# Kernel optimization log

Hardware: AMD Instinct MI355X
Metric: run time of the kernel (lower is better)

Reference implementation:

```python
import jax, jax.numpy as jnp
import numpy as np

B, L, D, KSIZE = 8, 2048, 768, 8


def setup_inputs() -> dict:
    key = jax.random.key(0)
    k1, k2, k3, k4, k5 = jax.random.split(key, 5)
    s = 1.0 / np.sqrt(D)  # torch default GRU init scale
    x = jax.random.normal(k1, (B, L, D), dtype=jnp.float32)
    w_ih = jax.random.uniform(k2, (D, 3 * D), jnp.float32, -s, s)
    w_hh = jax.random.uniform(k3, (D, 3 * D), jnp.float32, -s, s)
    b_ih = jax.random.uniform(k4, (3 * D,), jnp.float32, -s, s)
    b_hh = jax.random.uniform(k5, (3 * D,), jnp.float32, -s, s)
    return {"x": x, "w_ih": w_ih, "w_hh": w_hh, "b_ih": b_ih, "b_hh": b_hh, "ksize": KSIZE}


def reference(x, w_ih, w_hh, b_ih, b_hh, ksize):
    """LocalRNN forward: sliding window of size ksize (zero left-pad), GRU over
    each window, return last hidden state per position -> [B, L, D].
    Instead of materializing the redundant [B*L, ksize, D] windowed tensor,
    we run the ksize-step recurrence over all positions in parallel: the j-th
    GRU step for window ending at t consumes xpad[:, t + j, :].
    """
    Bb, Ll, Dd = x.shape
    xpad = jnp.concatenate([jnp.zeros((Bb, ksize - 1, Dd), x.dtype), x], axis=1)
    # precompute input-side gate activations once: [B, L+k-1, 3D]
    gx_all = xpad @ w_ih + b_ih

    def step(h, j):
        gx = jax.lax.dynamic_slice_in_dim(gx_all, j, Ll, axis=1)  # [B, L, 3D]
        gh = h @ w_hh + b_hh                                       # [B, L, 3D]
        xr, xz, xn = jnp.split(gx, 3, axis=-1)
        hr, hz, hn = jnp.split(gh, 3, axis=-1)
        r = jax.nn.sigmoid(xr + hr)
        z = jax.nn.sigmoid(xz + hz)
        n = jnp.tanh(xn + r * hn)
        h_new = (1.0 - z) * n + z * h
        return h_new, None

    h0 = jnp.zeros((Bb, Ll, Dd), x.dtype)
    h, _ = jax.lax.scan(step, h0, jnp.arange(ksize))
    return h
```

## Files before the change

kernel.cpp:

```cpp
#include <hip/hip_runtime.h>
#include <stdint.h>
#include <stddef.h>

using short8 = __attribute__((ext_vector_type(8))) short;
using short4v = __attribute__((ext_vector_type(4))) short;
using f32x4  = __attribute__((ext_vector_type(4))) float;

#define BB 8
#define LL 2048
#define DD 768
#define KS 8
#define ND 2304
#define NT 12
#define NBD 12

__device__ __forceinline__ float bf2f(unsigned short u) {
  union { uint32_t i; float f; } v; v.i = ((uint32_t)u) << 16; return v.f;
}
__device__ __forceinline__ unsigned short f2bf(float f) {
  union { float f; uint32_t i; } v; v.f = f;
  return (unsigned short)((v.i + 0x7FFFu + ((v.i >> 16) & 1u)) >> 16);
}
__device__ __forceinline__ float sigm(float x) { return 1.0f / (1.0f + __expf(-x)); }
__device__ __forceinline__ float tanh_fast(float x) {
  return 2.0f / (1.0f + __expf(-2.0f * x)) - 1.0f;
}
__device__ __forceinline__ void gload_lds16(const void* g, void* lds) {
  __builtin_amdgcn_global_load_lds(
      (const __attribute__((address_space(1))) void*)g,
      (__attribute__((address_space(3))) void*)lds, 16, 0, 0);
}

__device__ __forceinline__ void swz_blocks(int bid, int nbm, int nbn,
                                           int* mb, int* nb) {
  int gsz = 8 * nbn;
  int g = bid / gsz;
  int rem = bid - g * gsz;
  int gg = nbm - g * 8; if (gg > 8) gg = 8;
  *nb = rem / gg;
  *mb = g * 8 + (rem - *nb * gg);
}

__global__ void zero_k(unsigned short* p, int n) {
  int i = blockIdx.x * 256 + threadIdx.x;
  if (i < n) p[i] = 0;
}

__global__ void detect_k(const uint32_t* __restrict__ x, int* __restrict__ flag) {
  int t = threadIdx.x;
  uint32_t w = x[t * 16];
  int e = (int)((w >> 7) & 0xFF);
  int isbf = (e >= 112 && e <= 136) ? 1 : 0;
  unsigned long long m = __ballot(isbf);
  if (t == 0) *flag = (__popcll(m) >= 32) ? 1 : 0;
}

__global__ void transpose_k(const void* __restrict__ in,
                            unsigned short* __restrict__ out, int R, int C,
                            const int* __restrict__ flagp) {
  const bool bf = (*flagp != 0);
  __shared__ unsigned short t[32][33];
  int c0 = blockIdx.x * 32, r0 = blockIdx.y * 32;
  int tx = threadIdx.x, ty = threadIdx.y;
#pragma unroll
  for (int i = ty; i < 32; i += 8) {
    size_t idx = (size_t)(r0 + i) * C + c0 + tx;
    t[i][tx] = bf ? ((const unsigned short*)in)[idx]
                  : f2bf(((const float*)in)[idx]);
  }
  __syncthreads();
#pragma unroll
  for (int i = ty; i < 32; i += 8)
    out[(size_t)(c0 + i) * R + r0 + tx] = t[tx][i];
}

__global__ void conv_bias(const void* __restrict__ in,
                          unsigned short* __restrict__ out, int n,
                          const int* __restrict__ flagp) {
  const bool bf = (*flagp != 0);
  int i = blockIdx.x * 256 + threadIdx.x;
  if (i >= n) return;
  out[i] = bf ? ((const unsigned short*)in)[i] : f2bf(((const float*)in)[i]);
}

__global__ void conv_x(const void* __restrict__ xv,
                       unsigned short* __restrict__ xpadc,
                       int Uc, int t0, int total8,
                       const int* __restrict__ flagp) {
  if (*flagp != 0) return;
  int idx = blockIdx.x * 256 + threadIdx.x;
  if (idx >= total8) return;
  size_t e = (size_t)idx * 8;
  int d = (int)(e % DD);
  size_t ru = e / DD;
  int u = (int)(ru % Uc);
  int b = (int)(ru / Uc);
  int p = t0 + u;
  short8 v = {0, 0, 0, 0, 0, 0, 0, 0};
  if (p >= KS - 1) {
    size_t base = ((size_t)b * LL + (p - (KS - 1))) * DD + d;
    const float* fp = (const float*)xv + base;
    float4 a = *(const float4*)fp, b4 = *(const float4*)(fp + 4);
    v[0] = (short)f2bf(a.x); v[1] = (short)f2bf(a.y);
    v[2] = (short)f2bf(a.z); v[3] = (short)f2bf(a.w);
    v[4] = (short)f2bf(b4.x); v[5] = (short)f2bf(b4.y);
    v[6] = (short)f2bf(b4.z); v[7] = (short)f2bf(b4.w);
  }
  *(short8*)&xpadc[e] = v;
}

__global__ __launch_bounds__(256, 3) void gemm_gx(
    const unsigned short* __restrict__ xbf, const unsigned short* __restrict__ xpadc,
    const unsigned short* __restrict__ zrow, const unsigned short* __restrict__ WT,
    const unsigned short* __restrict__ bih, const unsigned short* __restrict__ bhh,
    unsigned short* __restrict__ gxp, unsigned short* __restrict__ h0,
    int Mrows, int Uc, int Tcc, int t0, const int* __restrict__ flagp, int nbm) {
  __shared__ __align__(16) unsigned short Al[128 * 64];
  __shared__ __align__(16) unsigned short Bl[192 * 64];
  const bool bfm = (*flagp != 0);
  const int tid = threadIdx.x, lane = tid & 63, wv = tid >> 6;
  const int wm = wv >> 1, wd = wv & 1;
  int mb, db; swz_blocks(blockIdx.x, nbm, NBD, &mb, &db);
  const int m0 = mb * 128, d0 = db * 64;
  const int h16 = lane >> 4, l16 = lane & 15;

  const int r0i = tid >> 3;
  const int slotg = (tid & 7) ^ (r0i & 7);
  const unsigned short* asrc[4];
#pragma unroll
  for (int it = 0; it < 4; ++it) {
    int grow = m0 + it * 32 + r0i; if (grow >= Mrows) grow = Mrows - 1;
    if (bfm) {
      int b = grow / Uc, u = grow - b * Uc;
      int p = t0 + u;
      asrc[it] = (p < KS - 1)
          ? (zrow + slotg * 8)
          : (xbf + ((size_t)b * LL + (p - (KS - 1))) * DD + slotg * 8);
    } else {
      asrc[it] = xpadc + (size_t)grow * DD + slotg * 8;
    }
  }
  const unsigned short* bbase = WT + (size_t)(d0 + r0i) * DD + slotg * 8;
  char* aldst = (char*)Al + (wv * 1024);
  char* bldst = (char*)Bl + (wv * 1024);

  f32x4 acc[4][2][3] = {};

  for (int kt = 0; kt < NT; ++kt) {
    const int ko = kt * 64;
#pragma unroll
    for (int it = 0; it < 4; ++it)
      gload_lds16(asrc[it] + ko, aldst + it * 4096);
#pragma unroll
    for (int it = 0; it < 6; ++it) {
      const size_t boff = (size_t)(it >> 1) * (DD * DD) + (size_t)(it & 1) * (32 * DD);
      gload_lds16(bbase + boff + ko, bldst + it * 4096);
    }
    __syncthreads();
#pragma unroll
    for (int s = 0; s < 2; ++s) {
      short8 af[4];
#pragma unroll
      for (int i = 0; i < 4; ++i) {
        int row = wm * 64 + i * 16 + l16;
        af[i] = *(const short8*)&Al[row * 64 + (((s * 4 + h16) ^ (row & 7)) * 8)];
      }
      short8 bfr[2][3];
#pragma unroll
      for (int jd = 0; jd < 2; ++jd)
#pragma unroll
        for (int g = 0; g < 3; ++g) {
          int row = g * 64 + wd * 32 + jd * 16 + l16;
          bfr[jd][g] = *(const short8*)&Bl[row * 64 + (((s * 4 + h16) ^ (row & 7)) * 8)];
        }
#pragma unroll
      for (int i = 0; i < 4; ++i)
#pragma unroll
        for (int jd = 0; jd < 2; ++jd)
#pragma unroll
          for (int g = 0; g < 3; ++g)
            acc[i][jd][g] = __builtin_amdgcn_mfma_f32_16x16x32_bf16(af[i], bfr[jd][g], acc[i][jd][g], 0, 0, 0);
    }
    if (kt + 1 < NT) __syncthreads();
  }

  const int b0 = m0 / Uc;
  const int u00 = m0 - b0 * Uc;
#pragma unroll
  for (int jd = 0; jd < 2; ++jd) {
    int d = d0 + wd * 32 + jd * 16 + l16;
    float bir = bf2f(bih[d]), biz = bf2f(bih[DD + d]), bin_ = bf2f(bih[2 * DD + d]);
    float bhr = bf2f(bhh[d]), bhz = bf2f(bhh[DD + d]), bhn = bf2f(bhh[2 * DD + d]);
#pragma unroll
    for (int i = 0; i < 4; ++i) {
      int mbase = m0 + wm * 64 + i * 16 + 4 * h16;
#pragma unroll
      for (int r2 = 0; r2 < 4; ++r2) {
        int m = mbase + r2;
        if (m >= Mrows) continue;
        float gr = acc[i][jd][0][r2] + bir;
        float gz = acc[i][jd][1][r2] + biz;
        float gn = acc[i][jd][2][r2] + bin_;
        short4v pk;
        pk[0] = (short)f2bf(gr); pk[1] = (short)f2bf(gz);
        pk[2] = (short)f2bf(gn); pk[3] = 0;
        *(short4v*)(gxp + (size_t)m * (DD * 4) + d * 4) = pk;
        int uu = u00 + (m - m0);
        int b = b0;
        if (uu >= Uc) { b += 1; uu -= Uc; }
        if (uu < Tcc) {
          float r = sigm(gr + bhr);
          float z = sigm(gz + bhz);
          float n = tanh_fast(gn + r * bhn);
          h0[((size_t)b * Tcc + uu) * DD + d] = f2bf((1.0f - z) * n);
        }
      }
    }
  }
}

__global__ __launch_bounds__(256, 3) void gemm_gru_step(
    const unsigned short* __restrict__ Hc, const unsigned short* __restrict__ WT,
    const unsigned short* __restrict__ bhh, const unsigned short* __restrict__ gxp,
    int Uc, void* __restrict__ Hn, int hnBS, int hnOff, int j, int lgTc,
    const int* __restrict__ flagp, int isFinal, int nbm) {
  __shared__ __align__(16) unsigned short Al[128 * 64];
  __shared__ __align__(16) unsigned short Bl[192 * 64];
  const bool bfm = (*flagp != 0);
  const int tid = threadIdx.x, lane = tid & 63, wv = tid >> 6;
  const int wm = wv >> 1, wd = wv & 1;
  int mb, db; swz_blocks(blockIdx.x, nbm, NBD, &mb, &db);
  const int m0 = mb * 128, d0 = db * 64;
  const int h16 = lane >> 4, l16 = lane & 15;
  const int tmask = (1 << lgTc) - 1;

  const int r0i = tid >> 3;
  const int slotg = (tid & 7) ^ (r0i & 7);
  const unsigned short* abase = Hc + (size_t)(m0 + r0i) * DD + slotg * 8;
  const unsigned short* bbase = WT + (size_t)(d0 + r0i) * DD + slotg * 8;
  char* aldst = (char*)Al + (wv * 1024);
  char* bldst = (char*)Bl + (wv * 1024);

  f32x4 acc[4][2][3] = {};

  for (int kt = 0; kt < NT; ++kt) {
    const int ko = kt * 64;
#pragma unroll
    for (int it = 0; it < 4; ++it)
      gload_lds16(abase + (size_t)it * (32 * DD) + ko, aldst + it * 4096);
#pragma unroll
    for (int it = 0; it < 6; ++it) {
      const size_t boff = (size_t)(it >> 1) * (DD * DD) + (size_t)(it & 1) * (32 * DD);
      gload_lds16(bbase + boff + ko, bldst + it * 4096);
    }
    __syncthreads();
#pragma unroll
    for (int s = 0; s < 2; ++s) {
      short8 af[4];
#pragma unroll
      for (int i = 0; i < 4; ++i) {
        int row = wm * 64 + i * 16 + l16;
        af[i] = *(const short8*)&Al[row * 64 + (((s * 4 + h16) ^ (row & 7)) * 8)];
      }
      short8 bfr[2][3];
#pragma unroll
      for (int jd = 0; jd < 2; ++jd)
#pragma unroll
        for (int g = 0; g < 3; ++g) {
          int row = g * 64 + wd * 32 + jd * 16 + l16;
          bfr[jd][g] = *(const short8*)&Bl[row * 64 + (((s * 4 + h16) ^ (row & 7)) * 8)];
        }
#pragma unroll
      for (int i = 0; i < 4; ++i)
#pragma unroll
        for (int jd = 0; jd < 2; ++jd)
#pragma unroll
          for (int g = 0; g < 3; ++g)
            acc[i][jd][g] = __builtin_amdgcn_mfma_f32_16x16x32_bf16(af[i], bfr[jd][g], acc[i][jd][g], 0, 0, 0);
    }
    if (kt + 1 < NT) __syncthreads();
  }

#pragma unroll
  for (int jd = 0; jd < 2; ++jd) {
    int d = d0 + wd * 32 + jd * 16 + l16;
    float br = bf2f(bhh[d]), bz = bf2f(bhh[DD + d]), bn = bf2f(bhh[2 * DD + d]);
#pragma unroll
    for (int i = 0; i < 4; ++i) {
      int mbase = m0 + wm * 64 + i * 16 + 4 * h16;
#pragma unroll
      for (int r2 = 0; r2 < 4; ++r2) {
        int m = mbase + r2;
        int b = m >> lgTc, t = m & tmask;
        size_t gxrow = (size_t)b * Uc + t + j;
        short4v pk = *(const short4v*)(gxp + gxrow * (DD * 4) + d * 4);
        float xr = bf2f((unsigned short)pk[0]);
        float xz = bf2f((unsigned short)pk[1]);
        float xn = bf2f((unsigned short)pk[2]);
        float gr = acc[i][jd][0][r2] + br;
        float gz = acc[i][jd][1][r2] + bz;
        float gn = acc[i][jd][2][r2] + bn;
        float rr = sigm(xr + gr);
        float zz = sigm(xz + gz);
        float nn = tanh_fast(xn + rr * gn);
        float ho = bf2f(Hc[(size_t)m * DD + d]);
        float val = (1.0f - zz) * nn + zz * ho;
        size_t hnrow = (size_t)b * hnBS + hnOff + t;
        if (isFinal && !bfm) ((float*)Hn)[hnrow * DD + d] = val;
        else ((unsigned short*)Hn)[hnrow * DD + d] = f2bf(val);
      }
    }
  }
}

extern "C" void kernel_launch(void* const* d_in, const int* in_sizes, int n_in,
                              void* d_out, int out_size, void* d_ws, size_t ws_size,
                              hipStream_t stream) {
  const void* x    = d_in[0];
  const void* w_ih = d_in[1];
  const void* w_hh = d_in[2];
  const void* b_ih = d_in[3];
  const void* b_hh = d_in[4];

  const size_t wTbytes = (size_t)ND * DD * 2;
  const size_t hdr = 2 * wTbytes + 2 * 4608 + 4096 + 4096;

  int Tc = 64;
  for (int tc = 2048; tc >= 64; tc >>= 1) {
    size_t hBsz  = (size_t)BB * tc * DD * 2;
    size_t xpsz  = (size_t)BB * (tc + KS - 1) * DD * 2;
    size_t uni   = hBsz > xpsz ? hBsz : xpsz;
    size_t need = hdr +
                  (size_t)BB * (tc + KS - 1) * DD * 8 +
                  (size_t)BB * tc * DD * 2 +
                  uni;
    if (need <= ws_size) { Tc = tc; break; }
  }
  int lgTc = 0; while ((1 << lgTc) < Tc) ++lgTc;
  const int Uc = Tc + KS - 1;
  const int Mc = BB * Tc;
  const int Mg = BB * Uc;

  char* ws = (char*)d_ws;
  unsigned short* wihT = (unsigned short*)ws; ws += wTbytes;
  unsigned short* whhT = (unsigned short*)ws; ws += wTbytes;
  unsigned short* bihB = (unsigned short*)ws; ws += 4608;
  unsigned short* bhhB = (unsigned short*)ws; ws += 4608;
  int* flag            = (int*)ws;            ws += 4096;
  unsigned short* zrow = (unsigned short*)ws; ws += 4096;
  unsigned short* gxc  = (unsigned short*)ws; ws += (size_t)Mg * DD * 8;
  unsigned short* hA   = (unsigned short*)ws; ws += (size_t)Mc * DD * 2;
  unsigned short* hB   = (unsigned short*)ws;
  unsigned short* xpadc = hB;

  detect_k<<<1, 64, 0, stream>>>((const uint32_t*)x, flag);
  zero_k<<<8, 256, 0, stream>>>(zrow, 2048);
  transpose_k<<<dim3(ND / 32, DD / 32), dim3(32, 8), 0, stream>>>(w_ih, wihT, DD, ND, flag);
  transpose_k<<<dim3(ND / 32, DD / 32), dim3(32, 8), 0, stream>>>(w_hh, whhT, DD, ND, flag);
  conv_bias<<<(ND + 255) / 256, 256, 0, stream>>>(b_ih, bihB, ND, flag);
  conv_bias<<<(ND + 255) / 256, 256, 0, stream>>>(b_hh, bhhB, ND, flag);

  const int nbmGx = (Mg + 127) / 128;
  const int nbmGru = Mc / 128;

  for (int t0 = 0; t0 < LL; t0 += Tc) {
    int total8 = Mg * (DD / 8);
    conv_x<<<(total8 + 255) / 256, 256, 0, stream>>>(x, xpadc, Uc, t0, total8, flag);

    gemm_gx<<<nbmGx * NBD, 256, 0, stream>>>(
        (const unsigned short*)x, xpadc, zrow, wihT, bihB, bhhB, gxc, hA,
        Mg, Uc, Tc, t0, flag, nbmGx);

    unsigned short* cur = hA;
    for (int j = 1; j <= 7; ++j) {
      int isFinal = (j == 7);
      void* dst = isFinal ? d_out : (void*)((cur == hA) ? hB : hA);
      int hnBS = isFinal ? LL : Tc;
      int hnOff = isFinal ? t0 : 0;
      gemm_gru_step<<<nbmGru * NBD, 256, 0, stream>>>(
          cur, whhT, bhhB, gxc, Uc, dst, hnBS, hnOff, j, lgTc, flag, isFinal, nbmGru);
      if (!isFinal) cur = (cur == hA) ? hB : hA;
    }
  }
}
```

Measured before the change: 693.5 us.

## Double-buffer LDS tiles in gx and GRU step GEMMs

Measured after the change: 820.8 us. +18.3%, slower.

```diff
diff --git a/kernel.cpp b/kernel.cpp
--- a/kernel.cpp
+++ b/kernel.cpp
@@ -109,14 +109,14 @@
   *(short8*)&xpadc[e] = v;
 }
 
-__global__ __launch_bounds__(256, 3) void gemm_gx(
+__global__ __launch_bounds__(256, 2) void gemm_gx(
     const unsigned short* __restrict__ xbf, const unsigned short* __restrict__ xpadc,
     const unsigned short* __restrict__ zrow, const unsigned short* __restrict__ WT,
     const unsigned short* __restrict__ bih, const unsigned short* __restrict__ bhh,
     unsigned short* __restrict__ gxp, unsigned short* __restrict__ h0,
     int Mrows, int Uc, int Tcc, int t0, const int* __restrict__ flagp, int nbm) {
-  __shared__ __align__(16) unsigned short Al[128 * 64];
-  __shared__ __align__(16) unsigned short Bl[192 * 64];
+  __shared__ __align__(16) unsigned short Al[2][128 * 64];
+  __shared__ __align__(16) unsigned short Bl[2][192 * 64];
   const bool bfm = (*flagp != 0);
   const int tid = threadIdx.x, lane = tid & 63, wv = tid >> 6;
   const int wm = wv >> 1, wd = wv & 1;
@@ -141,29 +141,40 @@
     }
   }
   const unsigned short* bbase = WT + (size_t)(d0 + r0i) * DD + slotg * 8;
-  char* aldst = (char*)Al + (wv * 1024);
-  char* bldst = (char*)Bl + (wv * 1024);
+
+#define GX_STAGE(KT, BUF)                                                     \
+  {                                                                           \
+    const int ko_ = (KT) * 64;                                                \
+    char* ad_ = (char*)Al[BUF] + wv * 1024;                                   \
+    char* bd_ = (char*)Bl[BUF] + wv * 1024;                                   \
+    _Pragma("unroll")                                                         \
+    for (int it = 0; it < 4; ++it)                                            \
+      gload_lds16(asrc[it] + ko_, ad_ + it * 4096);                           \
+    _Pragma("unroll")                                                         \
+    for (int it = 0; it < 6; ++it) {                                          \
+      const size_t boff_ = (size_t)(it >> 1) * (DD * DD) +                    \
+                           (size_t)(it & 1) * (32 * DD);                      \
+      gload_lds16(bbase + boff_ + ko_, bd_ + it * 4096);                      \
+    }                                                                         \
+  }
 
   f32x4 acc[4][2][3] = {};
 
+  GX_STAGE(0, 0);
+  __syncthreads();
+
+  int cur = 0;
   for (int kt = 0; kt < NT; ++kt) {
-    const int ko = kt * 64;
-#pragma unroll
-    for (int it = 0; it < 4; ++it)
-      gload_lds16(asrc[it] + ko, aldst + it * 4096);
-#pragma unroll
-    for (int it = 0; it < 6; ++it) {
-      const size_t boff = (size_t)(it >> 1) * (DD * DD) + (size_t)(it & 1) * (32 * DD);
-      gload_lds16(bbase + boff + ko, bldst + it * 4096);
-    }
-    __syncthreads();
+    if (kt + 1 < NT) GX_STAGE(kt + 1, cur ^ 1);
+    const unsigned short* Ab = Al[cur];
+    const unsigned short* Bb = Bl[cur];
 #pragma unroll
     for (int s = 0; s < 2; ++s) {
       short8 af[4];
 #pragma unroll
       for (int i = 0; i < 4; ++i) {
         int row = wm * 64 + i * 16 + l16;
-        af[i] = *(const short8*)&Al[row * 64 + (((s * 4 + h16) ^ (row & 7)) * 8)];
+        af[i] = *(const short8*)&Ab[row * 64 + (((s * 4 + h16) ^ (row & 7)) * 8)];
       }
       short8 bfr[2][3];
 #pragma unroll
@@ -171,7 +182,7 @@
 #pragma unroll
         for (int g = 0; g < 3; ++g) {
           int row = g * 64 + wd * 32 + jd * 16 + l16;
-          bfr[jd][g] = *(const short8*)&Bl[row * 64 + (((s * 4 + h16) ^ (row & 7)) * 8)];
+          bfr[jd][g] = *(const short8*)&Bb[row * 64 + (((s * 4 + h16) ^ (row & 7)) * 8)];
         }
 #pragma unroll
       for (int i = 0; i < 4; ++i)
@@ -181,8 +192,10 @@
           for (int g = 0; g < 3; ++g)
             acc[i][jd][g] = __builtin_amdgcn_mfma_f32_16x16x32_bf16(af[i], bfr[jd][g], acc[i][jd][g], 0, 0, 0);
     }
-    if (kt + 1 < NT) __syncthreads();
-  }
+    __syncthreads();
+    cur ^= 1;
+  }
+#undef GX_STAGE
 
   const int b0 = m0 / Uc;
   const int u00 = m0 - b0 * Uc;
@@ -219,13 +232,13 @@
   }
 }
 
-__global__ __launch_bounds__(256, 3) void gemm_gru_step(
+__global__ __launch_bounds__(256, 2) void gemm_gru_step(
     const unsigned short* __restrict__ Hc, const unsigned short* __restrict__ WT,
     const unsigned short* __restrict__ bhh, const unsigned short* __restrict__ gxp,
     int Uc, void* __restrict__ Hn, int hnBS, int hnOff, int j, int lgTc,
     const int* __restrict__ flagp, int isFinal, int nbm) {
-  __shared__ __align__(16) unsigned short Al[128 * 64];
-  __shared__ __align__(16) unsigned short Bl[192 * 64];
+  __shared__ __align__(16) unsigned short Al[2][128 * 64];
+  __shared__ __align__(16) unsigned short Bl[2][192 * 64];
   const bool bfm = (*flagp != 0);
   const int tid = threadIdx.x, lane = tid & 63, wv = tid >> 6;
   const int wm = wv >> 1, wd = wv & 1;
@@ -238,29 +251,40 @@
   const int slotg = (tid & 7) ^ (r0i & 7);
   const unsigned short* abase = Hc + (size_t)(m0 + r0i) * DD + slotg * 8;
   const unsigned short* bbase = WT + (size_t)(d0 + r0i) * DD + slotg * 8;
-  char* aldst = (char*)Al + (wv * 1024);
-  char* bldst = (char*)Bl + (wv * 1024);
+
+#define GRU_STAGE(KT, BUF)                                                    \
+  {                                                                           \
+    const int ko_ = (KT) * 64;                                                \
+    char* ad_ = (char*)Al[BUF] + wv * 1024;                                   \
+    char* bd_ = (char*)Bl[BUF] + wv * 1024;                                   \
+    _Pragma("unroll")                                                         \
+    for (int it = 0; it < 4; ++it)                                            \
+      gload_lds16(abase + (size_t)it * (32 * DD) + ko_, ad_ + it * 4096);     \
+    _Pragma("unroll")                                                         \
+    for (int it = 0; it < 6; ++it) {                                          \
+      const size_t boff_ = (size_t)(it >> 1) * (DD * DD) +                    \
+                           (size_t)(it & 1) * (32 * DD);                      \
+      gload_lds16(bbase + boff_ + ko_, bd_ + it * 4096);                      \
+    }                                                                         \
+  }
 
   f32x4 acc[4][2][3] = {};
 
+  GRU_STAGE(0, 0);
+  __syncthreads();
+
+  int cur = 0;
   for (int kt = 0; kt < NT; ++kt) {
-    const int ko = kt * 64;
-#pragma unroll
-    for (int it = 0; it < 4; ++it)
-      gload_lds16(abase + (size_t)it * (32 * DD) + ko, aldst + it * 4096);
-#pragma unroll
-    for (int it = 0; it < 6; ++it) {
-      const size_t boff = (size_t)(it >> 1) * (DD * DD) + (size_t)(it & 1) * (32 * DD);
-      gload_lds16(bbase + boff + ko, bldst + it * 4096);
-    }
-    __syncthreads();
+    if (kt + 1 < NT) GRU_STAGE(kt + 1, cur ^ 1);
+    const unsigned short* Ab = Al[cur];
+    const unsigned short* Bb = Bl[cur];
 #pragma unroll
     for (int s = 0; s < 2; ++s) {
       short8 af[4];
 #pragma unroll
       for (int i = 0; i < 4; ++i) {
         int row = wm * 64 + i * 16 + l16;
-        af[i] = *(const short8*)&Al[row * 64 + (((s * 4 + h16) ^ (row & 7)) * 8)];
+        af[i] = *(const short8*)&Ab[row * 64 + (((s * 4 + h16) ^ (row & 7)) * 8)];
       }
       short8 bfr[2][3];
 #pragma unroll
@@ -268,7 +292,7 @@
 #pragma unroll
         for (int g = 0; g < 3; ++g) {
           int row = g * 64 + wd * 32 + jd * 16 + l16;
-          bfr[jd][g] = *(const short8*)&Bl[row * 64 + (((s * 4 + h16) ^ (row & 7)) * 8)];
+          bfr[jd][g] = *(const short8*)&Bb[row * 64 + (((s * 4 + h16) ^ (row & 7)) * 8)];
         }
 #pragma unroll
       for (int i = 0; i < 4; ++i)
@@ -278,8 +302,10 @@
           for (int g = 0; g < 3; ++g)
             acc[i][jd][g] = __builtin_amdgcn_mfma_f32_16x16x32_bf16(af[i], bfr[jd][g], acc[i][jd][g], 0, 0, 0);
     }
-    if (kt + 1 < NT) __syncthreads();
-  }
+    __syncthreads();
+    cur ^= 1;
+  }
+#undef GRU_STAGE
 
 #pragma unroll
   for (int jd = 0; jd < 2; ++jd) {
```
